# Kernel tuning notes

Measured on AMD Instinct MI355X. Metric: run time of the kernel, lower is better.

The kernel has to match this reference:

```python
import jax, jax.numpy as jnp
import numpy as np


def gcn_conv(x, W, b, src, dst, dinv_sqrt, n_nodes):
    # PyG GCNConv: h = X W; out_i = sum_j norm_ij * h_j + b, norm = d_i^-1/2 d_j^-1/2
    h = x @ W  # [N, out]
    norm = dinv_sqrt[src] * dinv_sqrt[dst]  # [E]
    msg = h[src] * norm[:, None]  # [E, out]
    out = jax.ops.segment_sum(msg, dst, num_segments=n_nodes)
    return out + b


def setup_inputs() -> dict:
    key = jax.random.key(0)
    ks = jax.random.split(key, 12)
    N, E, G = 50000, 400000, 512
    x = jax.random.normal(ks[0], (N, 3), dtype=jnp.float32)
    edge_index = jax.random.randint(ks[1], (2, E), 0, N, dtype=jnp.int64)
    batch = jnp.sort(jax.random.randint(ks[2], (N,), 0, G, dtype=jnp.int64))
    def lin(k, fin, fout):
        kw, kb = jax.random.split(k)
        s = 1.0 / np.sqrt(fin)
        return (jax.random.uniform(kw, (fin, fout), jnp.float32, -s, s),
                jax.random.uniform(kb, (fout,), jnp.float32, -s, s))
    W1, b1 = lin(ks[3], 3, 100)
    W2, b2 = lin(ks[4], 100, 200)
    W3, b3 = lin(ks[5], 200, 100)
    W4, b4 = lin(ks[6], 100, 1)
    return {"x": x, "edge_index": edge_index, "batch": batch, "num_graphs": G,
            "W1": W1, "b1": b1, "W2": W2, "b2": b2,
            "W3": W3, "b3": b3, "W4": W4, "b4": b4}


def reference(x, edge_index, batch, num_graphs, W1, b1, W2, b2, W3, b3, W4, b4):
    N = x.shape[0]
    loop = jnp.arange(N, dtype=edge_index.dtype)
    src = jnp.concatenate([edge_index[0], loop])  # self-loops added (GCNConv default)
    dst = jnp.concatenate([edge_index[1], loop])
    deg = jax.ops.segment_sum(jnp.ones_like(src, dtype=x.dtype), dst, num_segments=N)
    dinv_sqrt = deg ** -0.5  # deg >= 1 due to self-loops

    h = jax.nn.silu(gcn_conv(x, W1, b1, src, dst, dinv_sqrt, N))
    h = jax.nn.silu(gcn_conv(h, W2, b2, src, dst, dinv_sqrt, N))

    # global_mean_pool over `batch` segments
    sums = jax.ops.segment_sum(h, batch, num_segments=num_graphs)  # [G, 200]
    cnts = jax.ops.segment_sum(jnp.ones((N,), h.dtype), batch, num_segments=num_graphs)
    pooled = sums / jnp.maximum(cnts, 1.0)[:, None]

    h = jax.nn.silu(pooled @ W3 + b3)
    out = h @ W4 + b4  # [G, 1]
    return out.squeeze(-1)
```

## Files before the change

kernel.cpp:

```cpp
#include <hip/hip_runtime.h>
#include <math.h>

#define WF 64

__device__ __forceinline__ float silu_f(float v){ return v / (1.0f + expf(-v)); }

typedef __attribute__((ext_vector_type(8))) short bf16x8;
typedef __attribute__((ext_vector_type(4))) float f32x4;

__device__ __forceinline__ void bf16split(float v, unsigned short& h, unsigned short& l){
  unsigned int b = __float_as_uint(v);
  unsigned int hh = (b + 0x8000u) >> 16;
  float hf = __uint_as_float(hh << 16);
  float lo = v - hf;
  unsigned int bl = __float_as_uint(lo);
  h = (unsigned short)hh;
  l = (unsigned short)((bl + 0x8000u) >> 16);
}

__global__ __launch_bounds__(256) void k_count(const int* __restrict__ dst, int* __restrict__ cnt, int E){
  int e = blockIdx.x*blockDim.x + threadIdx.x;
  if (e < E) atomicAdd(&cnt[dst[e]], 1);
}

__global__ __launch_bounds__(256) void k_scan1(const int* __restrict__ cnt, int* __restrict__ rowstart, int* __restrict__ bsum, int N){
  __shared__ int s[256];
  int tid = threadIdx.x;
  int base = blockIdx.x*2048 + tid*8;
  int loc[8]; int tsum = 0;
#pragma unroll
  for (int j=0;j<8;++j){ int idx=base+j; int v = (idx<N)?cnt[idx]:0; loc[j]=tsum; tsum+=v; }
  s[tid]=tsum; __syncthreads();
  for (int off=1; off<256; off<<=1){
    int v = (tid>=off)? s[tid-off] : 0;
    __syncthreads();
    s[tid] += v;
    __syncthreads();
  }
  int texc = s[tid] - tsum;
  if (tid==255) bsum[blockIdx.x] = s[255];
#pragma unroll
  for (int j=0;j<8;++j){ int idx=base+j; if (idx<N) rowstart[idx] = texc + loc[j]; }
}

__global__ __launch_bounds__(256) void k_scan3(const int* __restrict__ bsum, const int* __restrict__ cnt,
                        const float* __restrict__ x,
                        int* __restrict__ rowstart, int* __restrict__ cursor,
                        float* __restrict__ dinv, float4* __restrict__ dxp,
                        int N, int E, int nb){
  __shared__ int boffs;
  int tid = threadIdx.x;
  int b = (blockIdx.x*blockDim.x) >> 11;
  if (tid < WF){
    int v = (tid < nb && tid < b) ? bsum[tid] : 0;
#pragma unroll
    for (int off=32; off; off>>=1) v += __shfl_down(v, off);
    if (tid==0) boffs = v;
  }
  __syncthreads();
  int idx = blockIdx.x*blockDim.x + tid;
  if (idx < N){
    int v = rowstart[idx] + boffs;
    rowstart[idx]=v; cursor[idx]=v;
    float di = rsqrtf((float)(cnt[idx]+1));
    dinv[idx] = di;
    float4 o;
    o.x = di;
    o.y = di*x[3*idx+0];
    o.z = di*x[3*idx+1];
    o.w = di*x[3*idx+2];
    dxp[idx] = o;
  }
  if (idx==0) rowstart[N]=E;
}

__global__ __launch_bounds__(256) void k_fill(const int* __restrict__ src, const int* __restrict__ dst,
                       int* __restrict__ cursor, int* __restrict__ colsrc, int E){
  int e = blockIdx.x*blockDim.x + threadIdx.x;
  if (e < E){
    int d = dst[e];
    int pos = atomicAdd(&cursor[d], 1);
    colsrc[pos] = src[e];
  }
}

__global__ __launch_bounds__(256) void k_wconv(const float* __restrict__ W2,
                       unsigned short* __restrict__ w2th, unsigned short* __restrict__ w2tl){
  int idx = blockIdx.x*blockDim.x + threadIdx.x;
  if (idx < 224*128){
    int f = idx >> 7, k = idx & 127;
    float v = (f < 200 && k < 100) ? W2[(size_t)k*200 + f] : 0.f;
    unsigned short h, l;
    bf16split(v, h, l);
    w2th[idx] = h;
    w2tl[idx] = l;
  }
}

__global__ __launch_bounds__(256) void k_l1(const float4* __restrict__ dxp,
                     const int* __restrict__ rowstart, const int* __restrict__ colsrc,
                     const float* __restrict__ W1, const float* __restrict__ b1,
                     float* __restrict__ h1s, int N){
  __shared__ float w[300];
  __shared__ float bb[100];
  int tid = threadIdx.x;
  for (int t=tid; t<300; t+=blockDim.x) w[t]=W1[t];
  for (int t=tid; t<100; t+=blockDim.x) bb[t]=b1[t];
  __syncthreads();
  int i = blockIdx.x*blockDim.x + tid;
  if (i >= N) return;
  float4 self = dxp[i];
  float di = self.x;
  float sx = self.y, sy = self.z, sz = self.w;
  int jb = rowstart[i], je = rowstart[i+1];
  int j = jb;
  for (; j+3 < je; j += 4){
    float4 r0 = dxp[colsrc[j]];
    float4 r1 = dxp[colsrc[j+1]];
    float4 r2 = dxp[colsrc[j+2]];
    float4 r3 = dxp[colsrc[j+3]];
    sx += (r0.y + r1.y) + (r2.y + r3.y);
    sy += (r0.z + r1.z) + (r2.z + r3.z);
    sz += (r0.w + r1.w) + (r2.w + r3.w);
  }
  for (; j < je; ++j){
    float4 r = dxp[colsrc[j]];
    sx += r.y; sy += r.z; sz += r.w;
  }
  sx*=di; sy*=di; sz*=di;
  float* orow = h1s + (size_t)i*100;
#pragma unroll
  for (int f0=0; f0<100; f0+=4){
    float4 o;
    o.x = silu_f(sx*w[f0+0] + sy*w[100+f0+0] + sz*w[200+f0+0] + bb[f0+0]);
    o.y = silu_f(sx*w[f0+1] + sy*w[100+f0+1] + sz*w[200+f0+1] + bb[f0+1]);
    o.z = silu_f(sx*w[f0+2] + sy*w[100+f0+2] + sz*w[200+f0+2] + bb[f0+2]);
    o.w = silu_f(sx*w[f0+3] + sy*w[100+f0+3] + sz*w[200+f0+3] + bb[f0+3]);
    *(float4*)&orow[f0] = o;
  }
}

__global__ __launch_bounds__(256) void k_agg2(const float* __restrict__ h1s, const int* __restrict__ rowstart,
                       const int* __restrict__ colsrc, const float* __restrict__ dinv,
                       unsigned short* __restrict__ a2h, unsigned short* __restrict__ a2l, int N){
  int node = blockIdx.x*8 + (threadIdx.x >> 5);
  int lane = threadIdx.x & 31;
  if (node >= N) return;
  if (lane >= 25){
    int ko = 100 + (lane-25)*4;
    ushort4 z = make_ushort4(0,0,0,0);
    *(ushort4*)(a2h + (size_t)node*128 + ko) = z;
    *(ushort4*)(a2l + (size_t)node*128 + ko) = z;
    return;
  }
  float di = dinv[node];
  float4 v = *(const float4*)(h1s + (size_t)node*100 + lane*4);
  float4 acc;
  acc.x = di*v.x; acc.y = di*v.y; acc.z = di*v.z; acc.w = di*v.w;
  int jb = rowstart[node], je = rowstart[node+1];
  int j = jb;
  for (; j+1 < je; j += 2){
    int u0 = colsrc[j];   float w0 = dinv[u0];
    int u1 = colsrc[j+1]; float w1 = dinv[u1];
    float4 r0 = *(const float4*)(h1s + (size_t)u0*100 + lane*4);
    float4 r1 = *(const float4*)(h1s + (size_t)u1*100 + lane*4);
    acc.x += w0*r0.x + w1*r1.x;
    acc.y += w0*r0.y + w1*r1.y;
    acc.z += w0*r0.z + w1*r1.z;
    acc.w += w0*r0.w + w1*r1.w;
  }
  if (j < je){
    int u = colsrc[j]; float wv = dinv[u];
    float4 r = *(const float4*)(h1s + (size_t)u*100 + lane*4);
    acc.x += wv*r.x; acc.y += wv*r.y; acc.z += wv*r.z; acc.w += wv*r.w;
  }
  float o[4] = { di*acc.x, di*acc.y, di*acc.z, di*acc.w };
  ushort4 h4, l4;
  bf16split(o[0], h4.x, l4.x);
  bf16split(o[1], h4.y, l4.y);
  bf16split(o[2], h4.z, l4.z);
  bf16split(o[3], h4.w, l4.w);
  *(ushort4*)(a2h + (size_t)node*128 + lane*4) = h4;
  *(ushort4*)(a2l + (size_t)node*128 + lane*4) = l4;
}

__global__ __launch_bounds__(128) void k_mm2(const unsigned short* __restrict__ a2h,
                      const unsigned short* __restrict__ a2l,
                      const unsigned short* __restrict__ w2th,
                      const unsigned short* __restrict__ w2tl,
                      const float* __restrict__ b2, const int* __restrict__ batch,
                      float* __restrict__ pooled, int N, int nwg){
  __shared__ float plL[8*224];
  int tid = threadIdx.x;
  int l = tid & 63, w = tid >> 6;
  int orig = blockIdx.x;
  int q = nwg >> 3, r = nwg & 7;
  int xcd = orig % 8, rk = orig / 8;
  int bid = (xcd < r) ? (xcd*(q+1) + rk) : (r*(q+1) + (xcd-r)*q + rk);
  int n0 = bid * 32;
  int row = l & 15;
  int kg  = l >> 4;

  const unsigned short* ah_p = a2h + (size_t)(n0 + w*16 + row)*128;
  const unsigned short* al_p = a2l + (size_t)(n0 + w*16 + row)*128;

  bf16x8 ahf[4], alf[4];
#pragma unroll
  for (int ks = 0; ks < 4; ++ks){
    int ko = ks*32 + kg*8;
    ahf[ks] = *(const bf16x8*)(ah_p + ko);
    alf[ks] = *(const bf16x8*)(al_p + ko);
  }

  f32x4 accs[14];
#pragma unroll
  for (int i=0;i<14;++i) accs[i] = (f32x4){0.f,0.f,0.f,0.f};

#pragma unroll
  for (int fb = 0; fb < 7; ++fb){
    int gf0 = fb*32 + row, gf1 = gf0 + 16;
    const unsigned short* wh0_p = w2th + (size_t)gf0*128;
    const unsigned short* wl0_p = w2tl + (size_t)gf0*128;
    const unsigned short* wh1_p = w2th + (size_t)gf1*128;
    const unsigned short* wl1_p = w2tl + (size_t)gf1*128;
    f32x4 a0 = accs[2*fb], a1 = accs[2*fb+1];
#pragma unroll
    for (int ks = 0; ks < 4; ++ks){
      int ko = ks*32 + kg*8;
      bf16x8 wh0 = *(const bf16x8*)(wh0_p + ko);
      bf16x8 wl0 = *(const bf16x8*)(wl0_p + ko);
      bf16x8 wh1 = *(const bf16x8*)(wh1_p + ko);
      bf16x8 wl1 = *(const bf16x8*)(wl1_p + ko);
      a0 = __builtin_amdgcn_mfma_f32_16x16x32_bf16(ahf[ks], wh0, a0, 0, 0, 0);
      a0 = __builtin_amdgcn_mfma_f32_16x16x32_bf16(ahf[ks], wl0, a0, 0, 0, 0);
      a0 = __builtin_amdgcn_mfma_f32_16x16x32_bf16(alf[ks], wh0, a0, 0, 0, 0);
      a1 = __builtin_amdgcn_mfma_f32_16x16x32_bf16(ahf[ks], wh1, a1, 0, 0, 0);
      a1 = __builtin_amdgcn_mfma_f32_16x16x32_bf16(ahf[ks], wl1, a1, 0, 0, 0);
      a1 = __builtin_amdgcn_mfma_f32_16x16x32_bf16(alf[ks], wh1, a1, 0, 0, 0);
    }
    accs[2*fb] = a0; accs[2*fb+1] = a1;
  }

  for (int idx = tid; idx < 8*224; idx += 128) plL[idx] = 0.f;
  __syncthreads();

  int g0 = batch[n0];
#pragma unroll
  for (int ft = 0; ft < 14; ++ft){
    f32x4 a = accs[ft];
    int gf = (ft >> 1)*32 + (ft & 1)*16 + row;
    if (gf < 200){
      float bias = b2[gf];
      float s = 0.f;
      int gprev = -1;
#pragma unroll
      for (int r2 = 0; r2 < 4; ++r2){
        int node = n0 + w*16 + kg*4 + r2;
        if (node < N){
          int g = batch[node];
          if (g != gprev){
            if (gprev >= 0){
              int dg = gprev - g0;
              if (dg < 8) atomicAdd(&plL[dg*224 + gf], s);
              else        atomicAdd(&pooled[(size_t)gprev*200 + gf], s);
            }
            gprev = g; s = 0.f;
          }
          s += silu_f(a[r2] + bias);
        }
      }
      if (gprev >= 0){
        int dg = gprev - g0;
        if (dg < 8) atomicAdd(&plL[dg*224 + gf], s);
        else        atomicAdd(&pooled[(size_t)gprev*200 + gf], s);
      }
    }
  }
  __syncthreads();
  for (int idx = tid; idx < 8*224; idx += 128){
    float v = plL[idx];
    if (v != 0.f){
      int r2 = idx / 224, f = idx - r2*224;
      if (f < 200) atomicAdd(&pooled[(size_t)(g0+r2)*200 + f], v);
    }
  }
}

__global__ __launch_bounds__(256) void k_head(const float* __restrict__ pooled, const int* __restrict__ batch,
                       const float* __restrict__ W3, const float* __restrict__ b3,
                       const float* __restrict__ W4, const float* __restrict__ b4,
                       float* __restrict__ out, int N){
  __shared__ float pl[200];
  __shared__ float h3[100];
  int g = blockIdx.x; int tid = threadIdx.x;
  int lo=0, hi=N;
  while (lo<hi){ int m=(lo+hi)>>1; if (batch[m] < g) lo=m+1; else hi=m; }
  int s = lo;
  hi=N;
  while (lo<hi){ int m=(lo+hi)>>1; if (batch[m] < g+1) lo=m+1; else hi=m; }
  int e = lo;
  float inv = (e>s) ? 1.0f/(float)(e-s) : 0.0f;
  if (tid < 200) pl[tid] = pooled[(size_t)g*200 + tid] * inv;
  __syncthreads();
  if (tid < 100){
    float acc = b3[tid];
    for (int k=0;k<200;++k) acc += pl[k]*W3[k*100+tid];
    h3[tid] = silu_f(acc);
  }
  __syncthreads();
  if (tid < WF){
    float p = 0.f;
    if (tid < 100)      p  = h3[tid]     * W4[tid];
    if (tid + 64 < 100) p += h3[tid+64]  * W4[tid+64];
#pragma unroll
    for (int off=32; off; off>>=1) p += __shfl_down(p, off);
    if (tid==0) out[g] = p + b4[0];
  }
}

extern "C" void kernel_launch(void* const* d_in, const int* in_sizes, int n_in,
                              void* d_out, int out_size, void* d_ws, size_t ws_size,
                              hipStream_t stream){
  const float* x  = (const float*)d_in[0];
  const int*   ei = (const int*)  d_in[1];
  const int* batch= (const int*)  d_in[2];
  const float* W1 = (const float*)d_in[4];
  const float* b1 = (const float*)d_in[5];
  const float* W2 = (const float*)d_in[6];
  const float* b2 = (const float*)d_in[7];
  const float* W3 = (const float*)d_in[8];
  const float* b3 = (const float*)d_in[9];
  const float* W4 = (const float*)d_in[10];
  const float* b4 = (const float*)d_in[11];
  float* out = (float*)d_out;

  int N = in_sizes[0]/3;
  int E = in_sizes[1]/2;
  int G = out_size;
  const int* src = ei;
  const int* dst = ei + E;
  int NP = ((N + 63)/64)*64;

  char* base = (char*)d_ws; size_t off = 0;
  auto alloc = [&](size_t bytes)->void*{
    void* p = base + off;
    off = (off + bytes + 255) & ~(size_t)255;
    return p;
  };
  int*   cnt      = (int*)  alloc((size_t)N*4);
  float* pooled   = (float*)alloc((size_t)G*200*4);
  size_t zbytes   = off;
  int*   rowstart = (int*)  alloc((size_t)(N+1)*4);
  int*   cursor   = (int*)  alloc((size_t)N*4);
  int*   bsum     = (int*)  alloc(4096);
  int*   colsrc   = (int*)  alloc((size_t)E*4);
  float* dinv     = (float*)alloc((size_t)N*4);
  float4* dxp     = (float4*)alloc((size_t)N*16);
  float* h1s      = (float*)alloc((size_t)N*100*4);
  unsigned short* a2h = (unsigned short*)alloc((size_t)NP*128*2);
  unsigned short* a2l = (unsigned short*)alloc((size_t)NP*128*2);
  unsigned short* w2th = (unsigned short*)alloc((size_t)224*128*2);
  unsigned short* w2tl = (unsigned short*)alloc((size_t)224*128*2);
  (void)ws_size; (void)n_in;

  hipMemsetAsync(base, 0, zbytes, stream);
  int gE = (E+255)/256;
  k_count<<<gE,256,0,stream>>>(dst, cnt, E);
  int nb = (N+2047)/2048;
  k_scan1<<<nb,256,0,stream>>>(cnt, rowstart, bsum, N);
  k_scan3<<<(N+255)/256,256,0,stream>>>(bsum, cnt, x, rowstart, cursor, dinv, dxp, N, E, nb);
  k_wconv<<<(224*128+255)/256,256,0,stream>>>(W2, w2th, w2tl);
  k_fill<<<gE,256,0,stream>>>(src, dst, cursor, colsrc, E);
  k_l1<<<(N+255)/256,256,0,stream>>>(dxp, rowstart, colsrc, W1, b1, h1s, N);
  k_agg2<<<(N+7)/8,256,0,stream>>>(h1s, rowstart, colsrc, dinv, a2h, a2l, N);
  int nwg = (N+31)/32;
  k_mm2<<<nwg,128,0,stream>>>(a2h, a2l, w2th, w2tl, b2, batch, pooled, N, nwg);
  k_head<<<G,256,0,stream>>>(pooled, batch, W3, b3, W4, b4, out, N);
}
```

Before: 184.8 us.

## Write layer-2 activations to memory and pool them in the head kernel

The matmul kernel no longer does the mean-pool reduction with shared and global atomics. It writes the full SiLU layer-2 activations (N×200 floats) to a new buffer, and the head kernel sums each graph's rows serially per feature before the MLP. This removes the atomics and the shared-memory reduction in k_mm2, but adds a 40 MB write and read-back. It also makes the pooling in k_head a serial loop over about 100 nodes per graph.

Result: slower. 200.1 us (+8.3%).

```diff
diff --git a/kernel.cpp b/kernel.cpp
--- a/kernel.cpp
+++ b/kernel.cpp
@@ -188,9 +188,8 @@
                       const unsigned short* __restrict__ a2l,
                       const unsigned short* __restrict__ w2th,
                       const unsigned short* __restrict__ w2tl,
-                      const float* __restrict__ b2, const int* __restrict__ batch,
-                      float* __restrict__ pooled, int N, int nwg){
-  __shared__ float plL[8*224];
+                      const float* __restrict__ b2,
+                      float* __restrict__ h2s, int N, int nwg){
   int tid = threadIdx.x;
   int l = tid & 63, w = tid >> 6;
   int orig = blockIdx.x;
@@ -212,10 +211,6 @@
     alf[ks] = *(const bf16x8*)(al_p + ko);
   }
 
-  f32x4 accs[14];
-#pragma unroll
-  for (int i=0;i<14;++i) accs[i] = (f32x4){0.f,0.f,0.f,0.f};
-
 #pragma unroll
   for (int fb = 0; fb < 7; ++fb){
     int gf0 = fb*32 + row, gf1 = gf0 + 16;
@@ -223,7 +218,8 @@
     const unsigned short* wl0_p = w2tl + (size_t)gf0*128;
     const unsigned short* wh1_p = w2th + (size_t)gf1*128;
     const unsigned short* wl1_p = w2tl + (size_t)gf1*128;
-    f32x4 a0 = accs[2*fb], a1 = accs[2*fb+1];
+    f32x4 a0 = {0.f,0.f,0.f,0.f};
+    f32x4 a1 = {0.f,0.f,0.f,0.f};
 #pragma unroll
     for (int ks = 0; ks < 4; ++ks){
       int ko = ks*32 + kg*8;
@@ -238,55 +234,23 @@
       a1 = __builtin_amdgcn_mfma_f32_16x16x32_bf16(ahf[ks], wl1, a1, 0, 0, 0);
       a1 = __builtin_amdgcn_mfma_f32_16x16x32_bf16(alf[ks], wh1, a1, 0, 0, 0);
     }
-    accs[2*fb] = a0; accs[2*fb+1] = a1;
-  }
-
-  for (int idx = tid; idx < 8*224; idx += 128) plL[idx] = 0.f;
-  __syncthreads();
-
-  int g0 = batch[n0];
-#pragma unroll
-  for (int ft = 0; ft < 14; ++ft){
-    f32x4 a = accs[ft];
-    int gf = (ft >> 1)*32 + (ft & 1)*16 + row;
-    if (gf < 200){
-      float bias = b2[gf];
-      float s = 0.f;
-      int gprev = -1;
-#pragma unroll
-      for (int r2 = 0; r2 < 4; ++r2){
-        int node = n0 + w*16 + kg*4 + r2;
-        if (node < N){
-          int g = batch[node];
-          if (g != gprev){
-            if (gprev >= 0){
-              int dg = gprev - g0;
-              if (dg < 8) atomicAdd(&plL[dg*224 + gf], s);
-              else        atomicAdd(&pooled[(size_t)gprev*200 + gf], s);
-            }
-            gprev = g; s = 0.f;
-          }
-          s += silu_f(a[r2] + bias);
+#pragma unroll
+    for (int ft = 0; ft < 2; ++ft){
+      f32x4 a = ft ? a1 : a0;
+      int gf = fb*32 + ft*16 + row;
+      if (gf < 200){
+        float bias = b2[gf];
+#pragma unroll
+        for (int r2 = 0; r2 < 4; ++r2){
+          int node = n0 + w*16 + kg*4 + r2;
+          if (node < N) h2s[(size_t)node*200 + gf] = silu_f(a[r2] + bias);
         }
       }
-      if (gprev >= 0){
-        int dg = gprev - g0;
-        if (dg < 8) atomicAdd(&plL[dg*224 + gf], s);
-        else        atomicAdd(&pooled[(size_t)gprev*200 + gf], s);
-      }
     }
   }
-  __syncthreads();
-  for (int idx = tid; idx < 8*224; idx += 128){
-    float v = plL[idx];
-    if (v != 0.f){
-      int r2 = idx / 224, f = idx - r2*224;
-      if (f < 200) atomicAdd(&pooled[(size_t)(g0+r2)*200 + f], v);
-    }
-  }
-}
-
-__global__ __launch_bounds__(256) void k_head(const float* __restrict__ pooled, const int* __restrict__ batch,
+}
+
+__global__ __launch_bounds__(256) void k_head(const float* __restrict__ h2s, const int* __restrict__ batch,
                        const float* __restrict__ W3, const float* __restrict__ b3,
                        const float* __restrict__ W4, const float* __restrict__ b4,
                        float* __restrict__ out, int N){
@@ -300,7 +264,11 @@
   while (lo<hi){ int m=(lo+hi)>>1; if (batch[m] < g+1) lo=m+1; else hi=m; }
   int e = lo;
   float inv = (e>s) ? 1.0f/(float)(e-s) : 0.0f;
-  if (tid < 200) pl[tid] = pooled[(size_t)g*200 + tid] * inv;
+  if (tid < 200){
+    float acc=0.f;
+    for (int n=s; n<e; ++n) acc += h2s[(size_t)n*200 + tid];
+    pl[tid] = acc*inv;
+  }
   __syncthreads();
   if (tid < 100){
     float acc = b3[tid];
@@ -348,7 +316,6 @@
     return p;
   };
   int*   cnt      = (int*)  alloc((size_t)N*4);
-  float* pooled   = (float*)alloc((size_t)G*200*4);
   size_t zbytes   = off;
   int*   rowstart = (int*)  alloc((size_t)(N+1)*4);
   int*   cursor   = (int*)  alloc((size_t)N*4);
@@ -357,6 +324,7 @@
   float* dinv     = (float*)alloc((size_t)N*4);
   float4* dxp     = (float4*)alloc((size_t)N*16);
   float* h1s      = (float*)alloc((size_t)N*100*4);
+  float* h2s      = (float*)alloc((size_t)N*200*4);
   unsigned short* a2h = (unsigned short*)alloc((size_t)NP*128*2);
   unsigned short* a2l = (unsigned short*)alloc((size_t)NP*128*2);
   unsigned short* w2th = (unsigned short*)alloc((size_t)224*128*2);
@@ -374,6 +342,6 @@
   k_l1<<<(N+255)/256,256,0,stream>>>(dxp, rowstart, colsrc, W1, b1, h1s, N);
   k_agg2<<<(N+7)/8,256,0,stream>>>(h1s, rowstart, colsrc, dinv, a2h, a2l, N);
   int nwg = (N+31)/32;
-  k_mm2<<<nwg,128,0,stream>>>(a2h, a2l, w2th, w2tl, b2, batch, pooled, N, nwg);
-  k_head<<<G,256,0,stream>>>(pooled, batch, W3, b3, W4, b4, out, N);
-}
+  k_mm2<<<nwg,128,0,stream>>>(a2h, a2l, w2th, w2tl, b2, h2s, N, nwg);
+  k_head<<<G,256,0,stream>>>(h2s, batch, W3, b3, W4, b4, out, N);
+}
```
